# Kernel optimization log

Hardware: AMD Instinct MI355X
Metric: run time of the kernel (lower is better)

The kernel has to match this reference:

```python
import jax, jax.numpy as jnp
import numpy as np


def setup_inputs() -> dict:
    key = jax.random.key(0)
    k1, k2 = jax.random.split(key)
    B, R1, R2, D = 8, 4096, 4096, 128
    matrix_1 = jax.random.normal(k1, (B, R1, D), dtype=jnp.float32)
    matrix_2 = jax.random.normal(k2, (B, R2, D), dtype=jnp.float32)
    return {"matrix_1": matrix_1, "matrix_2": matrix_2}


def reference(matrix_1, matrix_2):
    # DotProductSimilarity over broadcast-tiled matrices == batched matmul.
    # (b, r1, d) x (b, r2, d) -> (b, r1, r2)
    return jnp.einsum('bid,bjd->bij', matrix_1, matrix_2)
```

## Files before the change

kernel.cpp:

```cpp
#include <hip/hip_runtime.h>
#include <stdint.h>


#define M_DIM 4096
#define N_DIM 4096
#define K_DIM 128

typedef __bf16  bf16x8 __attribute__((ext_vector_type(8)));
typedef float   f32x4  __attribute__((ext_vector_type(4)));

__device__ static inline unsigned short f2bf(float x) {
  union { float f; unsigned int u; } v; v.f = x;
  unsigned int u = v.u;
  unsigned int r = u + 0x7fffu + ((u >> 16) & 1u);
  return (unsigned short)(r >> 16);
}

__global__ __launch_bounds__(256) void cvt_kernel(const float* __restrict__ in,
                                                  unsigned short* __restrict__ out,
                                                  int n ) {
  int i = blockIdx.x * 256 + threadIdx.x;
  int n8 = n >> 3;
  if (i >= n8) return;
  const float4* p = (const float4*)in;
  float4 a = p[2 * i];
  float4 b = p[2 * i + 1];
  uint4 o;
  o.x = (unsigned)f2bf(a.x) | ((unsigned)f2bf(a.y) << 16);
  o.y = (unsigned)f2bf(a.z) | ((unsigned)f2bf(a.w) << 16);
  o.z = (unsigned)f2bf(b.x) | ((unsigned)f2bf(b.y) << 16);
  o.w = (unsigned)f2bf(b.z) | ((unsigned)f2bf(b.w) << 16);
  ((uint4*)out)[i] = o;
}

__device__ static inline void gl_lds16(const void* g, void* l) {
  __builtin_amdgcn_global_load_lds(
      (const __attribute__((address_space(1))) unsigned int*)g,
      (__attribute__((address_space(3))) unsigned int*)l,
      16, 0, 0);
}

__global__ __launch_bounds__(256) void gemm_bt_bf16(const unsigned short* __restrict__ A,
                                                    const unsigned short* __restrict__ Bm,
                                                    float* __restrict__ C) {
  __shared__ unsigned short As[128 * 32];
  __shared__ unsigned short Bs[128 * 32];

  const int tid  = threadIdx.x;
  const int lane = tid & 63;
  const int wid  = tid >> 6;
  const int wm   = wid >> 1;
  const int wn   = wid & 1;

  const int bz = blockIdx.z;
  const int bm = blockIdx.y * 128;
  const int bn = blockIdx.x * 128;

  const unsigned short* Ab = A  + (size_t)bz * M_DIM * K_DIM;
  const unsigned short* Bb = Bm + (size_t)bz * N_DIM * K_DIM;
  float*                Cb = C  + (size_t)bz * M_DIM * N_DIM;

  f32x4 acc[4][4] = {};

  const int mrow = lane & 15;
  const int kg   = lane >> 4;

  for (int k0 = 0; k0 < K_DIM; k0 += 32) {
    #pragma unroll
    for (int t = 0; t < 2; ++t) {
      int chunk = t * 256 + tid;
      int row   = chunk >> 2;
      int q     = chunk & 3;
      gl_lds16(Ab + (size_t)(bm + row) * K_DIM + k0 + q * 8, (char*)As + chunk * 16);
      gl_lds16(Bb + (size_t)(bn + row) * K_DIM + k0 + q * 8, (char*)Bs + chunk * 16);
    }
    __syncthreads();

    bf16x8 af[4], bfr[4];
    #pragma unroll
    for (int mi = 0; mi < 4; ++mi)
      af[mi] = *(const bf16x8*)&As[(wm * 64 + mi * 16 + mrow) * 32 + kg * 8];
    #pragma unroll
    for (int ni = 0; ni < 4; ++ni)
      bfr[ni] = *(const bf16x8*)&Bs[(wn * 64 + ni * 16 + mrow) * 32 + kg * 8];

    #pragma unroll
    for (int mi = 0; mi < 4; ++mi)
      #pragma unroll
      for (int ni = 0; ni < 4; ++ni)
        acc[mi][ni] = __builtin_amdgcn_mfma_f32_16x16x32_bf16(af[mi], bfr[ni],
                                                              acc[mi][ni], 0, 0, 0);
    __syncthreads();
  }

  const int rbase = (lane >> 4) * 4;
  const int col   = lane & 15;
  #pragma unroll
  for (int mi = 0; mi < 4; ++mi) {
    #pragma unroll
    for (int ni = 0; ni < 4; ++ni) {
      int gr = bm + wm * 64 + mi * 16 + rbase;
      int gc = bn + wn * 64 + ni * 16 + col;
      float* cp = Cb + (size_t)gr * N_DIM + gc;
      #pragma unroll
      for (int t = 0; t < 4; ++t)
        cp[(size_t)t * N_DIM] = acc[mi][ni][t];
    }
  }
}

__global__ void gemm_f32_fallback(const float* __restrict__ A,
                                  const float* __restrict__ B,
                                  float* __restrict__ C) {
  __shared__ float As[16][128];
  __shared__ float Bs2[16][128];
  int tx = threadIdx.x, ty = threadIdx.y;
  int tid = ty * 16 + tx;
  int bz = blockIdx.z;
  int bm = blockIdx.y * 16, bn = blockIdx.x * 16;
  const float* Ab = A + (size_t)bz * M_DIM * K_DIM;
  const float* Bb = B + (size_t)bz * N_DIM * K_DIM;
  for (int i = tid; i < 16 * 128; i += 256) {
    int r = i >> 7, c = i & 127;
    As[r][c]  = Ab[(size_t)(bm + r) * K_DIM + c];
    Bs2[r][c] = Bb[(size_t)(bn + r) * K_DIM + c];
  }
  __syncthreads();
  float s = 0.f;
  #pragma unroll 8
  for (int k = 0; k < 128; ++k) s += As[ty][k] * Bs2[tx][k];
  C[(size_t)bz * M_DIM * N_DIM + (size_t)(bm + ty) * N_DIM + bn + tx] = s;
}

extern "C" void kernel_launch(void* const* d_in, const int* in_sizes, int n_in,
                              void* d_out, int out_size, void* d_ws, size_t ws_size,
                              hipStream_t stream) {
  const float* A  = (const float*)d_in[0];
  const float* Bm = (const float*)d_in[1];
  float*       C  = (float*)d_out;

  const size_t elems    = (size_t)8 * M_DIM * K_DIM;
  const size_t bf_bytes = elems * 2;

  if (ws_size >= 2 * bf_bytes) {
    unsigned short* Abf = (unsigned short*)d_ws;
    unsigned short* Bbf = (unsigned short*)((char*)d_ws + bf_bytes);
    int n8 = (int)(elems >> 3);
    cvt_kernel<<<(n8 + 255) / 256, 256, 0, stream>>>(A,  Abf, (int)elems);
    cvt_kernel<<<(n8 + 255) / 256, 256, 0, stream>>>(Bm, Bbf, (int)elems);
    dim3 grid(N_DIM / 128, M_DIM / 128, 8);
    gemm_bt_bf16<<<grid, 256, 0, stream>>>(Abf, Bbf, C);
  } else {
    dim3 grid(N_DIM / 16, M_DIM / 16, 8);
    gemm_f32_fallback<<<grid, dim3(16, 16), 0, stream>>>(A, Bm, C);
  }
}
```

Measured before the change: 547.9 us.

## Load full K tile into XOR-swizzled LDS once and merge conversion kernels

Each GEMM block now loads the entire K=128 slice of A and B into LDS at once, 64 KB total, using an XOR swizzle on the 16-byte chunk index. This removes the per-k-step barrier pairs and is meant to avoid LDS bank conflicts on the MFMA fragment reads. The two fp32-to-bf16 conversion launches are merged into one kernel to save a launch. The larger LDS footprint may lower blocks per CU and reduces overlap between loads and compute.

```diff
diff --git a/kernel.cpp b/kernel.cpp
--- a/kernel.cpp
+++ b/kernel.cpp
@@ -16,21 +16,31 @@
   return (unsigned short)(r >> 16);
 }
 
-__global__ __launch_bounds__(256) void cvt_kernel(const float* __restrict__ in,
-                                                  unsigned short* __restrict__ out,
-                                                  int n ) {
+__global__ __launch_bounds__(256) void cvt2_kernel(const float* __restrict__ inA,
+                                                   const float* __restrict__ inB,
+                                                   unsigned short* __restrict__ outA,
+                                                   unsigned short* __restrict__ outB,
+                                                   int n8 ) {
   int i = blockIdx.x * 256 + threadIdx.x;
-  int n8 = n >> 3;
-  if (i >= n8) return;
+  const float* in;
+  unsigned short* out;
+  int j = i;
+  if (i < n8) {
+    in = inA; out = outA;
+  } else {
+    j = i - n8;
+    if (j >= n8) return;
+    in = inB; out = outB;
+  }
   const float4* p = (const float4*)in;
-  float4 a = p[2 * i];
-  float4 b = p[2 * i + 1];
+  float4 a = p[2 * j];
+  float4 b = p[2 * j + 1];
   uint4 o;
   o.x = (unsigned)f2bf(a.x) | ((unsigned)f2bf(a.y) << 16);
   o.y = (unsigned)f2bf(a.z) | ((unsigned)f2bf(a.w) << 16);
   o.z = (unsigned)f2bf(b.x) | ((unsigned)f2bf(b.y) << 16);
   o.w = (unsigned)f2bf(b.z) | ((unsigned)f2bf(b.w) << 16);
-  ((uint4*)out)[i] = o;
+  ((uint4*)out)[j] = o;
 }
 
 __device__ static inline void gl_lds16(const void* g, void* l) {
@@ -43,8 +53,8 @@
 __global__ __launch_bounds__(256) void gemm_bt_bf16(const unsigned short* __restrict__ A,
                                                     const unsigned short* __restrict__ Bm,
                                                     float* __restrict__ C) {
-  __shared__ unsigned short As[128 * 32];
-  __shared__ unsigned short Bs[128 * 32];
+  __shared__ unsigned short As[128 * 128];
+  __shared__ unsigned short Bs[128 * 128];
 
   const int tid  = threadIdx.x;
   const int lane = tid & 63;
@@ -65,24 +75,29 @@
   const int mrow = lane & 15;
   const int kg   = lane >> 4;
 
-  for (int k0 = 0; k0 < K_DIM; k0 += 32) {
-    #pragma unroll
-    for (int t = 0; t < 2; ++t) {
-      int chunk = t * 256 + tid;
-      int row   = chunk >> 2;
-      int q     = chunk & 3;
-      gl_lds16(Ab + (size_t)(bm + row) * K_DIM + k0 + q * 8, (char*)As + chunk * 16);
-      gl_lds16(Bb + (size_t)(bn + row) * K_DIM + k0 + q * 8, (char*)Bs + chunk * 16);
-    }
-    __syncthreads();
+  #pragma unroll
+  for (int t = 0; t < 8; ++t) {
+    int chunk = t * 256 + tid;
+    int row   = chunk >> 4;
+    int q     = chunk & 15;
+    int qs    = q ^ (row & 7);
+    gl_lds16(Ab + (size_t)(bm + row) * K_DIM + qs * 8, (char*)As + chunk * 16);
+    gl_lds16(Bb + (size_t)(bn + row) * K_DIM + qs * 8, (char*)Bs + chunk * 16);
+  }
+  __syncthreads();
 
+  const int sx = (mrow & 7) << 3;
+  #pragma unroll
+  for (int kk = 0; kk < 4; ++kk) {
     bf16x8 af[4], bfr[4];
+    const int ko = (kk * 32) | (kg * 8);
+    const int ks = ko ^ sx;
     #pragma unroll
     for (int mi = 0; mi < 4; ++mi)
-      af[mi] = *(const bf16x8*)&As[(wm * 64 + mi * 16 + mrow) * 32 + kg * 8];
+      af[mi] = *(const bf16x8*)&As[(wm * 64 + mi * 16 + mrow) * 128 + ks];
     #pragma unroll
     for (int ni = 0; ni < 4; ++ni)
-      bfr[ni] = *(const bf16x8*)&Bs[(wn * 64 + ni * 16 + mrow) * 32 + kg * 8];
+      bfr[ni] = *(const bf16x8*)&Bs[(wn * 64 + ni * 16 + mrow) * 128 + ks];
 
     #pragma unroll
     for (int mi = 0; mi < 4; ++mi)
@@ -90,7 +105,6 @@
       for (int ni = 0; ni < 4; ++ni)
         acc[mi][ni] = __builtin_amdgcn_mfma_f32_16x16x32_bf16(af[mi], bfr[ni],
                                                               acc[mi][ni], 0, 0, 0);
-    __syncthreads();
   }
 
   const int rbase = (lane >> 4) * 4;
@@ -146,8 +160,8 @@
     unsigned short* Abf = (unsigned short*)d_ws;
     unsigned short* Bbf = (unsigned short*)((char*)d_ws + bf_bytes);
     int n8 = (int)(elems >> 3);
-    cvt_kernel<<<(n8 + 255) / 256, 256, 0, stream>>>(A,  Abf, (int)elems);
-    cvt_kernel<<<(n8 + 255) / 256, 256, 0, stream>>>(Bm, Bbf, (int)elems);
+    int total = 2 * n8;
+    cvt2_kernel<<<(total + 255) / 256, 256, 0, stream>>>(A, Bm, Abf, Bbf, n8);
     dim3 grid(N_DIM / 128, M_DIM / 128, 8);
     gemm_bt_bf16<<<grid, 256, 0, stream>>>(Abf, Bbf, C);
   } else {
```

Measured after the change: 558.7 us. About the same (+2.0%).
